# Optimization experiments

Hardware: AMD Instinct MI355X
Metric: run time of the kernel (lower is better)

## Reference

```python
import jax, jax.numpy as jnp
import numpy as np

N, S, D_MODEL, H = 2, 2048, 1024, 16
HEAD_DIM = D_MODEL // H


def setup_inputs() -> dict:
    key = jax.random.key(0)
    k1, k2, k3 = jax.random.split(key, 3)
    x = jax.random.normal(k1, (N, S, D_MODEL), dtype=jnp.float32)
    # Xavier-uniform-like scaling for the projection weights (torch layout: [out, in])
    lim_qkv = (6.0 / (D_MODEL + 3 * D_MODEL)) ** 0.5
    lim_o = (6.0 / (D_MODEL + D_MODEL)) ** 0.5
    qkv_w = jax.random.uniform(k2, (3 * D_MODEL, D_MODEL), dtype=jnp.float32, minval=-lim_qkv, maxval=lim_qkv)
    o_w = jax.random.uniform(k3, (D_MODEL, D_MODEL), dtype=jnp.float32, minval=-lim_o, maxval=lim_o)
    return {"x": x, "qkv_w": qkv_w, "o_w": o_w}


def reference(x, qkv_w, o_w):
    n, s, _ = x.shape
    # qkv projection (torch Linear: y = x @ W^T), no bias
    qkv = jnp.einsum("nsd,ed->nse", x, qkv_w)            # (N, S, 3*D_MODEL)
    qkv = qkv.reshape(n, s, H, 3 * HEAD_DIM).transpose(0, 2, 1, 3)  # (N, H, S, 3*hd)
    q, k, v = jnp.split(qkv, 3, axis=-1)                 # each (N, H, S, hd)
    scale = 1.0 / jnp.sqrt(jnp.float32(HEAD_DIM))
    attn_logits = jnp.einsum("nhqd,nhkd->nhqk", q, k) * scale  # (N, H, S, S)
    attn_weights = jax.nn.softmax(attn_logits, axis=-1)
    values = jnp.einsum("nhqk,nhkd->nhqd", attn_weights, v)    # (N, H, S, hd)
    values = values.transpose(0, 2, 1, 3).reshape(n, s, D_MODEL)
    o = jnp.einsum("nsd,ed->nse", values, o_w)           # (N, S, D_MODEL)
    return o
```

## Files before the change

kernel.cpp:

```cpp
#include <hip/hip_runtime.h>
#include <math.h>

#define H 16
#define S 2048
#define DM 1024
#define HD 64
#define QSCALE 0.18033688011112042f

typedef __attribute__((ext_vector_type(8))) short short8;
typedef __attribute__((ext_vector_type(4))) float f32x4;
typedef __attribute__((ext_vector_type(4))) unsigned short u16x4;
typedef __attribute__((ext_vector_type(2))) unsigned int uint2v;
#if __has_builtin(__builtin_amdgcn_cvt_pk_bf16_f32)
typedef __attribute__((ext_vector_type(2))) __bf16 bf16x2;
#endif

__device__ __forceinline__ unsigned short f2bf(float f) {
  unsigned int u = __builtin_bit_cast(unsigned int, f);
  u = (u + 0x7fffu + ((u >> 16) & 1u)) >> 16;
  return (unsigned short)u;
}

__device__ __forceinline__ unsigned int pk_bf16(float a, float b) {
#if __has_builtin(__builtin_amdgcn_cvt_pk_bf16_f32)
  bf16x2 r = __builtin_amdgcn_cvt_pk_bf16_f32(a, b);
  return __builtin_bit_cast(unsigned int, r);
#else
  return (unsigned int)f2bf(a) | ((unsigned int)f2bf(b) << 16);
#endif
}

__device__ __forceinline__ float fexp2(float x) {
#if __has_builtin(__builtin_amdgcn_exp2f)
  return __builtin_amdgcn_exp2f(x);
#else
  return exp2f(x);
#endif
}

__device__ __forceinline__ void async_ld16(const void* g, void* l) {
  __builtin_amdgcn_global_load_lds(
      (const __attribute__((address_space(1))) unsigned int*)g,
      (__attribute__((address_space(3))) unsigned int*)l, 16, 0, 0);
}

__global__ void convert_all(const float* __restrict__ x, const float* __restrict__ w,
                            const float* __restrict__ ow,
                            unsigned short* __restrict__ xb,
                            unsigned short* __restrict__ wb,
                            unsigned short* __restrict__ owb) {
  int b = blockIdx.x;
  const f32x4* src;
  u16x4* dst;
  int idx;
  if (b < 4096) {
    src = (const f32x4*)x; dst = (u16x4*)xb; idx = b * 256 + threadIdx.x;
  } else if (b < 7168) {
    src = (const f32x4*)w; dst = (u16x4*)wb; idx = (b - 4096) * 256 + threadIdx.x;
  } else {
    src = (const f32x4*)ow; dst = (u16x4*)owb; idx = (b - 7168) * 256 + threadIdx.x;
  }
  f32x4 v = src[idx];
  u16x4 r;
  r.x = f2bf(v.x); r.y = f2bf(v.y); r.z = f2bf(v.z); r.w = f2bf(v.w);
  dst[idx] = r;
}

__global__ __launch_bounds__(256, 2) void gemm_qkv(
    const short* __restrict__ X, const short* __restrict__ W,
    unsigned short* __restrict__ qws, unsigned short* __restrict__ kws,
    unsigned short* __restrict__ vtws) {
  const int K = 1024;
  __shared__ __attribute__((aligned(16))) short As[128 * 64];
  __shared__ __attribute__((aligned(16))) short Bs[96 * 64];
  const int tid = threadIdx.x;
  const int w = tid >> 6, l = tid & 63, l15 = l & 15, quad = l >> 4;
  const int wm = (w >> 1) * 64, wn = (w & 1) * 48;
  const int row0 = blockIdx.y * 128, col0 = blockIdx.x * 96;

  f32x4 zero = {0.f, 0.f, 0.f, 0.f};
  f32x4 acc[4][3];
  for (int i = 0; i < 4; ++i)
    for (int j = 0; j < 3; ++j) acc[i][j] = zero;

  const short* Ag = X + row0 * K;
  const short* Bg = W + col0 * K;

  for (int k0 = 0; k0 < K; k0 += 64) {
    __syncthreads();
    for (int i = 0; i < 4; ++i) {
      int u = i * 256 + tid;
      int r = u >> 3, c = u & 7;
      async_ld16(Ag + r * K + k0 + c * 8, As + u * 8);
    }
    for (int i = 0; i < 3; ++i) {
      int u = i * 256 + tid;
      int r = u >> 3, c = u & 7;
      async_ld16(Bg + r * K + k0 + c * 8, Bs + u * 8);
    }
    __syncthreads();
    for (int kk = 0; kk < 2; ++kk) {
      short8 a[4], b[3];
      for (int i = 0; i < 4; ++i)
        a[i] = *(const short8*)(As + (wm + i * 16 + l15) * 64 + kk * 32 + quad * 8);
      for (int j = 0; j < 3; ++j)
        b[j] = *(const short8*)(Bs + (wn + j * 16 + l15) * 64 + kk * 32 + quad * 8);
      for (int i = 0; i < 4; ++i)
        for (int j = 0; j < 3; ++j)
          acc[i][j] = __builtin_amdgcn_mfma_f32_16x16x32_bf16(a[i], b[j], acc[i][j], 0, 0, 0);
    }
  }

  for (int i = 0; i < 4; ++i) {
    int rowb = row0 + wm + i * 16 + quad * 4;
    int n = rowb >> 11, s = rowb & 2047;
    for (int j = 0; j < 3; ++j) {
      int e = col0 + wn + j * 16 + l15;
      int h = e / 192;
      int rem = e - h * 192;
      int part = rem >> 6, d = rem & 63;
      f32x4 v = acc[i][j];
      if (part == 0) {
        unsigned short* p = qws + ((n * H + h) * S + s) * HD + d;
        p[0] = f2bf(v.x * QSCALE);
        p[HD] = f2bf(v.y * QSCALE);
        p[2 * HD] = f2bf(v.z * QSCALE);
        p[3 * HD] = f2bf(v.w * QSCALE);
      } else if (part == 1) {
        unsigned short* p = kws + ((n * H + h) * S + s) * HD + d;
        p[0] = f2bf(v.x);
        p[HD] = f2bf(v.y);
        p[2 * HD] = f2bf(v.z);
        p[3 * HD] = f2bf(v.w);
      } else {
        u16x4 pk;
        pk.x = f2bf(v.x); pk.y = f2bf(v.y); pk.z = f2bf(v.z); pk.w = f2bf(v.w);
        *(u16x4*)(vtws + ((n * H + h) * HD + d) * S + s) = pk;
      }
    }
  }
}

__global__ __launch_bounds__(512, 4) void flash(
    const short* __restrict__ qws, const short* __restrict__ kws,
    const short* __restrict__ vtws, unsigned short* __restrict__ vals) {
  __shared__ __attribute__((aligned(16))) short Ks[2][128 * 64];
  __shared__ __attribute__((aligned(16))) short Vts[2][2][64 * 64];
  __shared__ __attribute__((aligned(16))) short Pt[8][16 * 64];
  const int tid = threadIdx.x;
  const int w = tid >> 6, l = tid & 63, l15 = l & 15, quad = l >> 4;
  const int qb = blockIdx.x, h = blockIdx.y, n = blockIdx.z;
  const int nh = n * H + h;
  const short* Qh = qws + nh * S * HD;
  const short* Kh = kws + nh * S * HD;
  const short* Vth = vtws + nh * HD * S;

  const int q0 = qb * 128 + w * 16;
  short8 qf[2];
  for (int c = 0; c < 2; ++c)
    qf[c] = *(const short8*)(Qh + (q0 + l15) * HD + c * 32 + quad * 8);

  const int swz0 = ((4 * 0 + quad) ^ (l15 & 7)) * 8;
  const int swz1 = ((4 * 1 + quad) ^ (l15 & 7)) * 8;

  float lpart = 0.f;
  f32x4 zero = {0.f, 0.f, 0.f, 0.f};
  f32x4 oacc[4] = {zero, zero, zero, zero};

  auto stage = [&](int kv0, int buf) {
    for (int i = 0; i < 2; ++i) {
      int u = i * 512 + tid;
      int r = u >> 3;
      int c = (u & 7) ^ (r & 7);
      async_ld16(Kh + (kv0 + r) * HD + c * 8, &Ks[buf][u * 8]);
    }
    for (int i = 0; i < 2; ++i) {
      int v = tid;
      int r = v >> 3;
      int c = (v & 7) ^ (r & 7);
      async_ld16(Vth + r * S + kv0 + i * 64 + c * 8, &Vts[buf][i][v * 8]);
    }
  };

  stage(0, 0);
  for (int t = 0; t < 16; ++t) {
    const int buf = t & 1;
    __syncthreads();
    if (t < 15) stage((t + 1) * 128, buf ^ 1);

    for (int ss = 0; ss < 2; ++ss) {
      const short* Kb = &Ks[buf][ss * 64 * 64];
      const short* Vb = Vts[buf][ss];

      f32x4 sacc[4] = {zero, zero, zero, zero};
      {
        short8 kf[4];
        for (int i = 0; i < 4; ++i)
          kf[i] = *(const short8*)(Kb + (i * 16 + l15) * 64 + swz0);
        for (int i = 0; i < 4; ++i)
          sacc[i] = __builtin_amdgcn_mfma_f32_16x16x32_bf16(kf[i], qf[0], sacc[i], 0, 0, 0);
        for (int i = 0; i < 4; ++i)
          kf[i] = *(const short8*)(Kb + (i * 16 + l15) * 64 + swz1);
        for (int i = 0; i < 4; ++i)
          sacc[i] = __builtin_amdgcn_mfma_f32_16x16x32_bf16(kf[i], qf[1], sacc[i], 0, 0, 0);
      }

      for (int i = 0; i < 4; ++i) {
        f32x4 p;
        p.x = fexp2(sacc[i].x);
        p.y = fexp2(sacc[i].y);
        p.z = fexp2(sacc[i].z);
        p.w = fexp2(sacc[i].w);
        sacc[i] = p;
        lpart += p.x + p.y + p.z + p.w;
      }

      for (int i = 0; i < 4; ++i) {
        int g = 2 * i + (quad >> 1);
        uint2v pk;
        pk.x = pk_bf16(sacc[i].x, sacc[i].y);
        pk.y = pk_bf16(sacc[i].z, sacc[i].w);
        *(uint2v*)(&Pt[w][l15 * 64 + ((g ^ (l15 & 7)) * 8) + (quad & 1) * 4]) = pk;
      }
      asm volatile("s_waitcnt lgkmcnt(0)" ::: "memory");

      {
        short8 vf[4];
        short8 pf0 = *(const short8*)(&Pt[w][l15 * 64 + swz0]);
        short8 pf1 = *(const short8*)(&Pt[w][l15 * 64 + swz1]);
        for (int i = 0; i < 4; ++i)
          vf[i] = *(const short8*)(Vb + (i * 16 + l15) * 64 + swz0);
        for (int i = 0; i < 4; ++i)
          oacc[i] = __builtin_amdgcn_mfma_f32_16x16x32_bf16(vf[i], pf0, oacc[i], 0, 0, 0);
        for (int i = 0; i < 4; ++i)
          vf[i] = *(const short8*)(Vb + (i * 16 + l15) * 64 + swz1);
        for (int i = 0; i < 4; ++i)
          oacc[i] = __builtin_amdgcn_mfma_f32_16x16x32_bf16(vf[i], pf1, oacc[i], 0, 0, 0);
      }
    }
  }

  float lrun = lpart;
  lrun += __shfl_xor(lrun, 16);
  lrun += __shfl_xor(lrun, 32);
  float inv = 1.0f / lrun;
  int s = q0 + l15;
  for (int i = 0; i < 4; ++i) {
    uint2v pk;
    pk.x = pk_bf16(oacc[i].x * inv, oacc[i].y * inv);
    pk.y = pk_bf16(oacc[i].z * inv, oacc[i].w * inv);
    *(uint2v*)(vals + (n * S + s) * DM + h * HD + i * 16 + quad * 4) = pk;
  }
}

__global__ __launch_bounds__(256, 2) void gemm_out(
    const short* __restrict__ A, const short* __restrict__ W,
    float* __restrict__ out) {
  const int K = 1024;
  __shared__ __attribute__((aligned(16))) short As[128 * 64];
  __shared__ __attribute__((aligned(16))) short Bs[64 * 64];
  const int tid = threadIdx.x;
  const int w = tid >> 6, l = tid & 63, l15 = l & 15, quad = l >> 4;
  const int wm = (w >> 1) * 64, wn = (w & 1) * 32;
  const int row0 = blockIdx.y * 128, col0 = blockIdx.x * 64;

  f32x4 zero = {0.f, 0.f, 0.f, 0.f};
  f32x4 acc[4][2];
  for (int i = 0; i < 4; ++i)
    for (int j = 0; j < 2; ++j) acc[i][j] = zero;

  const short* Ag = A + row0 * K;
  const short* Bg = W + col0 * K;

  for (int k0 = 0; k0 < K; k0 += 64) {
    __syncthreads();
    for (int i = 0; i < 4; ++i) {
      int u = i * 256 + tid;
      int r = u >> 3, c = u & 7;
      async_ld16(Ag + r * K + k0 + c * 8, As + u * 8);
    }
    for (int i = 0; i < 2; ++i) {
      int u = i * 256 + tid;
      int r = u >> 3, c = u & 7;
      async_ld16(Bg + r * K + k0 + c * 8, Bs + u * 8);
    }
    __syncthreads();
    for (int kk = 0; kk < 2; ++kk) {
      short8 a[4], b[2];
      for (int i = 0; i < 4; ++i)
        a[i] = *(const short8*)(As + (wm + i * 16 + l15) * 64 + kk * 32 + quad * 8);
      for (int j = 0; j < 2; ++j)
        b[j] = *(const short8*)(Bs + (wn + j * 16 + l15) * 64 + kk * 32 + quad * 8);
      for (int i = 0; i < 4; ++i)
        for (int j = 0; j < 2; ++j)
          acc[i][j] = __builtin_amdgcn_mfma_f32_16x16x32_bf16(a[i], b[j], acc[i][j], 0, 0, 0);
    }
  }

  for (int i = 0; i < 4; ++i) {
    int rowb = row0 + wm + i * 16 + quad * 4;
    for (int j = 0; j < 2; ++j) {
      int e = col0 + wn + j * 16 + l15;
      f32x4 v = acc[i][j];
      out[(rowb + 0) * 1024 + e] = v.x;
      out[(rowb + 1) * 1024 + e] = v.y;
      out[(rowb + 2) * 1024 + e] = v.z;
      out[(rowb + 3) * 1024 + e] = v.w;
    }
  }
}

extern "C" void kernel_launch(void* const* d_in, const int* in_sizes, int n_in,
                              void* d_out, int out_size, void* d_ws, size_t ws_size,
                              hipStream_t stream) {
  const float* x = (const float*)d_in[0];
  const float* qkv_w = (const float*)d_in[1];
  const float* o_w = (const float*)d_in[2];
  float* out = (float*)d_out;

  char* ws = (char*)d_ws;
  unsigned short* xb   = (unsigned short*)(ws);
  unsigned short* wb   = (unsigned short*)(ws + (8ull << 20));
  unsigned short* owb  = (unsigned short*)(ws + (14ull << 20));
  unsigned short* qws  = (unsigned short*)(ws + (16ull << 20));
  unsigned short* kws  = (unsigned short*)(ws + (24ull << 20));
  unsigned short* vtws = (unsigned short*)(ws + (32ull << 20));
  unsigned short* vals = xb;

  convert_all<<<8192, 256, 0, stream>>>(x, qkv_w, o_w, xb, wb, owb);
  gemm_qkv<<<dim3(32, 32), 256, 0, stream>>>(
      (const short*)xb, (const short*)wb, qws, kws, vtws);
  flash<<<dim3(16, 16, 2), 512, 0, stream>>>(
      (const short*)qws, (const short*)kws, (const short*)vtws, vals);
  gemm_out<<<dim3(16, 32), 256, 0, stream>>>(
      (const short*)vals, (const short*)owb, out);
}
```

Measured before the change: 190.7 us.

## Give each flash wave 32 query rows to reuse K/V fragments

The flash kernel drops from 8 waves of 16 query rows to 4 waves of 32 query rows per block. Each K and V fragment read from LDS now feeds two MFMAs, which halves LDS reads per FLOP. The staging loops are rewritten for 256 threads. In exchange each wave holds more registers (double accumulators), there are fewer waves per block, and occupancy drops (launch bounds 256,2), which may reduce latency hiding.

Measured after the change: 190.1 us. No clear change (-0.3%).

```diff
diff --git a/kernel.cpp b/kernel.cpp
--- a/kernel.cpp
+++ b/kernel.cpp
@@ -141,12 +141,12 @@
   }
 }
 
-__global__ __launch_bounds__(512, 4) void flash(
+__global__ __launch_bounds__(256, 2) void flash(
     const short* __restrict__ qws, const short* __restrict__ kws,
     const short* __restrict__ vtws, unsigned short* __restrict__ vals) {
   __shared__ __attribute__((aligned(16))) short Ks[2][128 * 64];
   __shared__ __attribute__((aligned(16))) short Vts[2][2][64 * 64];
-  __shared__ __attribute__((aligned(16))) short Pt[8][16 * 64];
+  __shared__ __attribute__((aligned(16))) short Pt[4][32 * 64];
   const int tid = threadIdx.x;
   const int w = tid >> 6, l = tid & 63, l15 = l & 15, quad = l >> 4;
   const int qb = blockIdx.x, h = blockIdx.y, n = blockIdx.z;
@@ -155,30 +155,35 @@
   const short* Kh = kws + nh * S * HD;
   const short* Vth = vtws + nh * HD * S;
 
-  const int q0 = qb * 128 + w * 16;
-  short8 qf[2];
+  const int q0 = qb * 128 + w * 32;
+  short8 qf[2][2];
   for (int c = 0; c < 2; ++c)
-    qf[c] = *(const short8*)(Qh + (q0 + l15) * HD + c * 32 + quad * 8);
+    for (int j = 0; j < 2; ++j)
+      qf[c][j] = *(const short8*)(Qh + (q0 + j * 16 + l15) * HD + c * 32 + quad * 8);
 
   const int swz0 = ((4 * 0 + quad) ^ (l15 & 7)) * 8;
   const int swz1 = ((4 * 1 + quad) ^ (l15 & 7)) * 8;
 
-  float lpart = 0.f;
+  float lpart[2] = {0.f, 0.f};
   f32x4 zero = {0.f, 0.f, 0.f, 0.f};
-  f32x4 oacc[4] = {zero, zero, zero, zero};
+  f32x4 oacc[4][2];
+  for (int i = 0; i < 4; ++i)
+    for (int j = 0; j < 2; ++j) oacc[i][j] = zero;
 
   auto stage = [&](int kv0, int buf) {
-    for (int i = 0; i < 2; ++i) {
-      int u = i * 512 + tid;
+    for (int i = 0; i < 4; ++i) {
+      int u = i * 256 + tid;
       int r = u >> 3;
       int c = (u & 7) ^ (r & 7);
       async_ld16(Kh + (kv0 + r) * HD + c * 8, &Ks[buf][u * 8]);
     }
-    for (int i = 0; i < 2; ++i) {
-      int v = tid;
-      int r = v >> 3;
-      int c = (v & 7) ^ (r & 7);
-      async_ld16(Vth + r * S + kv0 + i * 64 + c * 8, &Vts[buf][i][v * 8]);
+    for (int sub = 0; sub < 2; ++sub) {
+      for (int i = 0; i < 2; ++i) {
+        int u = i * 256 + tid;
+        int r = u >> 3;
+        int c = (u & 7) ^ (r & 7);
+        async_ld16(Vth + r * S + kv0 + sub * 64 + c * 8, &Vts[buf][sub][u * 8]);
+      }
     }
   };
 
@@ -192,64 +197,83 @@
       const short* Kb = &Ks[buf][ss * 64 * 64];
       const short* Vb = Vts[buf][ss];
 
-      f32x4 sacc[4] = {zero, zero, zero, zero};
+      f32x4 sacc[4][2];
+      for (int i = 0; i < 4; ++i)
+        for (int j = 0; j < 2; ++j) sacc[i][j] = zero;
       {
         short8 kf[4];
         for (int i = 0; i < 4; ++i)
           kf[i] = *(const short8*)(Kb + (i * 16 + l15) * 64 + swz0);
-        for (int i = 0; i < 4; ++i)
-          sacc[i] = __builtin_amdgcn_mfma_f32_16x16x32_bf16(kf[i], qf[0], sacc[i], 0, 0, 0);
+        for (int i = 0; i < 4; ++i) {
+          sacc[i][0] = __builtin_amdgcn_mfma_f32_16x16x32_bf16(kf[i], qf[0][0], sacc[i][0], 0, 0, 0);
+          sacc[i][1] = __builtin_amdgcn_mfma_f32_16x16x32_bf16(kf[i], qf[0][1], sacc[i][1], 0, 0, 0);
+        }
         for (int i = 0; i < 4; ++i)
           kf[i] = *(const short8*)(Kb + (i * 16 + l15) * 64 + swz1);
-        for (int i = 0; i < 4; ++i)
-          sacc[i] = __builtin_amdgcn_mfma_f32_16x16x32_bf16(kf[i], qf[1], sacc[i], 0, 0, 0);
+        for (int i = 0; i < 4; ++i) {
+          sacc[i][0] = __builtin_amdgcn_mfma_f32_16x16x32_bf16(kf[i], qf[1][0], sacc[i][0], 0, 0, 0);
+          sacc[i][1] = __builtin_amdgcn_mfma_f32_16x16x32_bf16(kf[i], qf[1][1], sacc[i][1], 0, 0, 0);
+        }
       }
 
       for (int i = 0; i < 4; ++i) {
-        f32x4 p;
-        p.x = fexp2(sacc[i].x);
-        p.y = fexp2(sacc[i].y);
-        p.z = fexp2(sacc[i].z);
-        p.w = fexp2(sacc[i].w);
-        sacc[i] = p;
-        lpart += p.x + p.y + p.z + p.w;
+        for (int j = 0; j < 2; ++j) {
+          f32x4 p;
+          p.x = fexp2(sacc[i][j].x);
+          p.y = fexp2(sacc[i][j].y);
+          p.z = fexp2(sacc[i][j].z);
+          p.w = fexp2(sacc[i][j].w);
+          sacc[i][j] = p;
+          lpart[j] += p.x + p.y + p.z + p.w;
+        }
       }
 
       for (int i = 0; i < 4; ++i) {
         int g = 2 * i + (quad >> 1);
-        uint2v pk;
-        pk.x = pk_bf16(sacc[i].x, sacc[i].y);
-        pk.y = pk_bf16(sacc[i].z, sacc[i].w);
-        *(uint2v*)(&Pt[w][l15 * 64 + ((g ^ (l15 & 7)) * 8) + (quad & 1) * 4]) = pk;
+        for (int j = 0; j < 2; ++j) {
+          uint2v pk;
+          pk.x = pk_bf16(sacc[i][j].x, sacc[i][j].y);
+          pk.y = pk_bf16(sacc[i][j].z, sacc[i][j].w);
+          *(uint2v*)(&Pt[w][(j * 16 + l15) * 64 + ((g ^ (l15 & 7)) * 8) + (quad & 1) * 4]) = pk;
+        }
       }
       asm volatile("s_waitcnt lgkmcnt(0)" ::: "memory");
 
       {
+        short8 pf[2][2];
+        pf[0][0] = *(const short8*)(&Pt[w][(0 * 16 + l15) * 64 + swz0]);
+        pf[0][1] = *(const short8*)(&Pt[w][(1 * 16 + l15) * 64 + swz0]);
+        pf[1][0] = *(const short8*)(&Pt[w][(0 * 16 + l15) * 64 + swz1]);
+        pf[1][1] = *(const short8*)(&Pt[w][(1 * 16 + l15) * 64 + swz1]);
         short8 vf[4];
-        short8 pf0 = *(const short8*)(&Pt[w][l15 * 64 + swz0]);
-        short8 pf1 = *(const short8*)(&Pt[w][l15 * 64 + swz1]);
         for (int i = 0; i < 4; ++i)
           vf[i] = *(const short8*)(Vb + (i * 16 + l15) * 64 + swz0);
-        for (int i = 0; i < 4; ++i)
-          oacc[i] = __builtin_amdgcn_mfma_f32_16x16x32_bf16(vf[i], pf0, oacc[i], 0, 0, 0);
+        for (int i = 0; i < 4; ++i) {
+          oacc[i][0] = __builtin_amdgcn_mfma_f32_16x16x32_bf16(vf[i], pf[0][0], oacc[i][0], 0, 0, 0);
+          oacc[i][1] = __builtin_amdgcn_mfma_f32_16x16x32_bf16(vf[i], pf[0][1], oacc[i][1], 0, 0, 0);
+        }
         for (int i = 0; i < 4; ++i)
           vf[i] = *(const short8*)(Vb + (i * 16 + l15) * 64 + swz1);
-        for (int i = 0; i < 4; ++i)
-          oacc[i] = __builtin_amdgcn_mfma_f32_16x16x32_bf16(vf[i], pf1, oacc[i], 0, 0, 0);
-      }
-    }
-  }
-
-  float lrun = lpart;
-  lrun += __shfl_xor(lrun, 16);
-  lrun += __shfl_xor(lrun, 32);
-  float inv = 1.0f / lrun;
-  int s = q0 + l15;
-  for (int i = 0; i < 4; ++i) {
-    uint2v pk;
-    pk.x = pk_bf16(oacc[i].x * inv, oacc[i].y * inv);
-    pk.y = pk_bf16(oacc[i].z * inv, oacc[i].w * inv);
-    *(uint2v*)(vals + (n * S + s) * DM + h * HD + i * 16 + quad * 4) = pk;
+        for (int i = 0; i < 4; ++i) {
+          oacc[i][0] = __builtin_amdgcn_mfma_f32_16x16x32_bf16(vf[i], pf[1][0], oacc[i][0], 0, 0, 0);
+          oacc[i][1] = __builtin_amdgcn_mfma_f32_16x16x32_bf16(vf[i], pf[1][1], oacc[i][1], 0, 0, 0);
+        }
+      }
+    }
+  }
+
+  for (int j = 0; j < 2; ++j) {
+    float lrun = lpart[j];
+    lrun += __shfl_xor(lrun, 16);
+    lrun += __shfl_xor(lrun, 32);
+    float inv = 1.0f / lrun;
+    int s = q0 + j * 16 + l15;
+    for (int i = 0; i < 4; ++i) {
+      uint2v pk;
+      pk.x = pk_bf16(oacc[i][j].x * inv, oacc[i][j].y * inv);
+      pk.y = pk_bf16(oacc[i][j].z * inv, oacc[i][j].w * inv);
+      *(uint2v*)(vals + (n * S + s) * DM + h * HD + i * 16 + quad * 4) = pk;
+    }
   }
 }
 
@@ -330,7 +354,7 @@
   convert_all<<<8192, 256, 0, stream>>>(x, qkv_w, o_w, xb, wb, owb);
   gemm_qkv<<<dim3(32, 32), 256, 0, stream>>>(
       (const short*)xb, (const short*)wb, qws, kws, vtws);
-  flash<<<dim3(16, 16, 2), 512, 0, stream>>>(
+  flash<<<dim3(16, 16, 2), 256, 0, stream>>>(
       (const short*)qws, (const short*)kws, (const short*)vtws, vals);
   gemm_out<<<dim3(16, 32), 256, 0, stream>>>(
       (const short*)vals, (const short*)owb, out);
```
